# Kernel optimization log

Measured on AMD Instinct MI355X. Metric: run time of the kernel, lower is better.

The kernel has to match this reference:

```python
import jax, jax.numpy as jnp
import numpy as np

D_HIDDEN = 1024
N_HEADS = 16
D_HEAD = 64
B, N = 4, 1024
EPS = 1e-5


def _lin(x, w, b):
    # torch Linear: y = x @ W^T + b, w: [out, in]
    return jnp.einsum('...i,oi->...o', x, w) + b


def _ln(x, g, b):
    m = jnp.mean(x, axis=-1, keepdims=True)
    v = jnp.mean(jnp.square(x - m), axis=-1, keepdims=True)
    return (x - m) * jax.lax.rsqrt(v + EPS) * g + b


def setup_inputs() -> dict:
    key = jax.random.key(0)
    ks = jax.random.split(key, 20)
    d = D_HIDDEN
    s = 0.02
    inp = {
        'x': jax.random.normal(ks[0], (B, N, d), jnp.float32),
        'time_emb': jax.random.normal(ks[1], (B, d), jnp.float32),
        'ln1_g': jnp.ones((d,), jnp.float32),
        'ln1_b': jnp.zeros((d,), jnp.float32),
        's1_w': jax.random.normal(ks[2], (d, d), jnp.float32) * s,
        's1_b': jnp.zeros((d,), jnp.float32),
        'o1_w': jax.random.normal(ks[3], (d, d), jnp.float32) * s,
        'o1_b': jnp.zeros((d,), jnp.float32),
        'qkv_w': jax.random.normal(ks[4], (3 * d, d), jnp.float32) * s,
        'qkv_b': jnp.zeros((3 * d,), jnp.float32),
        'proj_w': jax.random.normal(ks[5], (d, d), jnp.float32) * s,
        'proj_b': jnp.zeros((d,), jnp.float32),
        'ln2_g': jnp.ones((d,), jnp.float32),
        'ln2_b': jnp.zeros((d,), jnp.float32),
        's2_w': jax.random.normal(ks[6], (d, d), jnp.float32) * s,
        's2_b': jnp.zeros((d,), jnp.float32),
        'o2_w': jax.random.normal(ks[7], (d, d), jnp.float32) * s,
        'o2_b': jnp.zeros((d,), jnp.float32),
        'up_w': jax.random.normal(ks[8], (4 * d, d), jnp.float32) * s,
        'up_b': jnp.zeros((4 * d,), jnp.float32),
        'down_w': jax.random.normal(ks[9], (d, 4 * d), jnp.float32) * s,
        'down_b': jnp.zeros((d,), jnp.float32),
    }
    return inp


def reference(x, time_emb, ln1_g, ln1_b, s1_w, s1_b, o1_w, o1_b,
              qkv_w, qkv_b, proj_w, proj_b, ln2_g, ln2_b,
              s2_w, s2_b, o2_w, o2_b, up_w, up_b, down_w, down_b):
    d = D_HIDDEN

    def ada(h, sw, sb, ow, ob):
        scale = _lin(time_emb, sw, sb)[:, None, :]   # [B,1,d]
        offset = _lin(time_emb, ow, ob)[:, None, :]
        return (1.0 + scale) * h + offset

    # attention branch
    h = ada(_ln(x, ln1_g, ln1_b), s1_w, s1_b, o1_w, o1_b)
    qkv = _lin(h, qkv_w, qkv_b)                       # [B,N,3d]
    q, k, v = jnp.split(qkv, 3, axis=-1)
    q = q.reshape(B, N, N_HEADS, D_HEAD)
    k = k.reshape(B, N, N_HEADS, D_HEAD)
    v = v.reshape(B, N, N_HEADS, D_HEAD)
    wei = jnp.einsum('bnhd,bmhd->bhnm', q, k) * (D_HEAD ** -0.5)
    wei = jax.nn.softmax(wei, axis=-1)
    attn = jnp.einsum('bhnm,bmhd->bnhd', wei, v).reshape(B, N, d)
    x = x + _lin(attn, proj_w, proj_b)

    # mlp branch (torch nn.GELU default = exact erf gelu)
    h = ada(_ln(x, ln2_g, ln2_b), s2_w, s2_b, o2_w, o2_b)
    h = jax.nn.gelu(_lin(h, up_w, up_b), approximate=False)
    x = x + _lin(h, down_w, down_b)
    return x, time_emb
```

## Files before the change

kernel.cpp:

```cpp
#include <hip/hip_runtime.h>
#include <hip/hip_bf16.h>
#include <math.h>

#define DH 1024
#define BB 4
#define NN 1024
#define NH 16
#define HD 64

typedef __attribute__((ext_vector_type(8))) short bf16x8;
typedef __attribute__((ext_vector_type(4))) float f32x4;
typedef unsigned short u16;

static __device__ __forceinline__ u16 f2bf(float f) {
  __hip_bfloat16 h = __float2bfloat16(f);
  return *reinterpret_cast<u16*>(&h);
}
static __device__ __forceinline__ float bf2f(u16 x) {
  return __uint_as_float((unsigned)x << 16);
}

#define MFMA16(a, b, c) __builtin_amdgcn_mfma_f32_16x16x32_bf16(a, b, c, 0, 0, 0)
#define VMCNT(n) asm volatile("s_waitcnt vmcnt(" #n ")" ::: "memory")
#define MEMFENCE asm volatile("" ::: "memory")

static __device__ __forceinline__ void async16(const void* g, void* l) {
  __builtin_amdgcn_global_load_lds(
      (const __attribute__((address_space(1))) void*)g,
      (__attribute__((address_space(3))) void*)l, 16, 0, 0);
}

__global__ void cvt_all_kernel(const float* __restrict__ wq, const float* __restrict__ wp,
                               const float* __restrict__ wu, const float* __restrict__ wd,
                               u16* __restrict__ oq, u16* __restrict__ op,
                               u16* __restrict__ ou, u16* __restrict__ od) {
  int i = blockIdx.x * 256 + threadIdx.x;
  const float* src; u16* dst; int off;
  if (i < 786432)            { src = wq; dst = oq; off = i; }
  else if (i < 1048576)      { src = wp; dst = op; off = i - 786432; }
  else if (i < 2097152)      { src = wu; dst = ou; off = i - 1048576; }
  else                       { src = wd; dst = od; off = i - 2097152; }
  float4 v = reinterpret_cast<const float4*>(src)[off];
  ushort4 o;
  o.x = f2bf(v.x); o.y = f2bf(v.y); o.z = f2bf(v.z); o.w = f2bf(v.w);
  reinterpret_cast<ushort4*>(dst)[off] = o;
}

__global__ __launch_bounds__(256) void adaln_kernel(
    const float* __restrict__ e,
    const float* __restrict__ w_s1, const float* __restrict__ b_s1,
    const float* __restrict__ w_o1, const float* __restrict__ b_o1,
    const float* __restrict__ w_s2, const float* __restrict__ b_s2,
    const float* __restrict__ w_o2, const float* __restrict__ b_o2,
    float* __restrict__ out) {
  int tid = threadIdx.x, wid = tid >> 6, lane = tid & 63;
  int mat = blockIdx.y;
  const float* w; const float* bs; float addc;
  if (mat == 0)      { w = w_s1; bs = b_s1; addc = 1.f; }
  else if (mat == 1) { w = w_o1; bs = b_o1; addc = 0.f; }
  else if (mat == 2) { w = w_s2; bs = b_s2; addc = 1.f; }
  else               { w = w_o2; bs = b_o2; addc = 0.f; }
  int col = blockIdx.x * 4 + wid;
  float a0 = 0.f, a1 = 0.f, a2 = 0.f, a3 = 0.f;
  const float* wc_ = w + (size_t)col * DH;
  for (int i = 0; i < 16; ++i) {
    int k = i * 64 + lane;
    float wv = wc_[k];
    a0 += wv * e[k];
    a1 += wv * e[DH + k];
    a2 += wv * e[2 * DH + k];
    a3 += wv * e[3 * DH + k];
  }
  #pragma unroll
  for (int msk = 32; msk; msk >>= 1) {
    a0 += __shfl_xor(a0, msk); a1 += __shfl_xor(a1, msk);
    a2 += __shfl_xor(a2, msk); a3 += __shfl_xor(a3, msk);
  }
  if (lane == 0) {
    float bb = bs[col] + addc;
    out[mat * (4 * DH) + 0 * DH + col] = a0 + bb;
    out[mat * (4 * DH) + 1 * DH + col] = a1 + bb;
    out[mat * (4 * DH) + 2 * DH + col] = a2 + bb;
    out[mat * (4 * DH) + 3 * DH + col] = a3 + bb;
  }
}

__global__ __launch_bounds__(256) void ln_mod_kernel(
    const float* __restrict__ x, const float* __restrict__ g, const float* __restrict__ bta,
    const float* __restrict__ sp, const float* __restrict__ off, u16* __restrict__ out) {
  int row = blockIdx.x;
  int b = row >> 10;
  int tid = threadIdx.x;
  int wid = tid >> 6, lane = tid & 63;
  const float4 xv = reinterpret_cast<const float4*>(x + (size_t)row * DH)[tid];
  float s = xv.x + xv.y + xv.z + xv.w;
  float ss = xv.x * xv.x + xv.y * xv.y + xv.z * xv.z + xv.w * xv.w;
  #pragma unroll
  for (int m = 32; m; m >>= 1) { s += __shfl_xor(s, m); ss += __shfl_xor(ss, m); }
  __shared__ float red[8];
  if (lane == 0) { red[wid] = s; red[4 + wid] = ss; }
  __syncthreads();
  s = red[0] + red[1] + red[2] + red[3];
  ss = red[4] + red[5] + red[6] + red[7];
  float mean = s * (1.f / DH);
  float var = ss * (1.f / DH) - mean * mean;
  float rstd = rsqrtf(var + 1e-5f);
  int c = tid * 4;
  const float* spb = sp + b * DH + c;
  const float* offb = off + b * DH + c;
  float y0 = (xv.x - mean) * rstd * g[c + 0] + bta[c + 0];
  float y1 = (xv.y - mean) * rstd * g[c + 1] + bta[c + 1];
  float y2 = (xv.z - mean) * rstd * g[c + 2] + bta[c + 2];
  float y3 = (xv.w - mean) * rstd * g[c + 3] + bta[c + 3];
  ushort4 o;
  o.x = f2bf(spb[0] * y0 + offb[0]);
  o.y = f2bf(spb[1] * y1 + offb[1]);
  o.z = f2bf(spb[2] * y2 + offb[2]);
  o.w = f2bf(spb[3] * y3 + offb[3]);
  reinterpret_cast<ushort4*>(out + (size_t)row * DH)[tid] = o;
}

enum { EPI_BF16 = 0, EPI_GELU = 1, EPI_PART = 2 };

template <int EPI>
__global__ __launch_bounds__(512, 2) void gemm256_kernel(
    const u16* __restrict__ A, const u16* __restrict__ W,
    const float* __restrict__ bias, void* __restrict__ outp,
    int N, int K, int KT) {
  extern __shared__ u16 lds[];
  u16* Ab = lds;
  u16* Bb = lds + 32768;
  int tid = threadIdx.x;
  int wid = tid >> 6, lane = tid & 63;
  int l15 = lane & 15, l4 = lane >> 4;
  int wr = wid >> 2, wc = wid & 3;

  int nwg = gridDim.x * gridDim.y;
  int lin = blockIdx.y * gridDim.x + blockIdx.x;
  int q8 = nwg >> 3;
  int lin2 = (lin & 7) * q8 + (lin >> 3);
  int bx = lin2 % gridDim.x, by = lin2 / gridDim.x;
  int m0 = by * 256, n0 = bx * 256;
  int k0 = blockIdx.z * (KT << 5);

  f32x4 acc[8][4] = {};

  const u16* Abase = A + (size_t)m0 * K + k0;
  const u16* Wbase = W + (size_t)n0 * K + k0;
  int i0 = tid, i1 = 512 + tid;
  int r0 = i0 >> 2, c0 = (i0 & 3) ^ ((r0 >> 1) & 3);
  int r1 = i1 >> 2, c1 = (i1 & 3) ^ ((r1 >> 1) & 3);
  size_t gO0 = (size_t)r0 * K + c0 * 8;
  size_t gO1 = (size_t)r1 * K + c1 * 8;
  int lb0 = (wid * 64) * 8;
  int lb1 = (512 + wid * 64) * 8;

  auto stage = [&](int tt) {
    int q = (tt & 3) * 8192;
    const u16* Ak = Abase + tt * 32;
    const u16* Wk = Wbase + tt * 32;
    async16(Ak + gO0, &Ab[q + lb0]);
    async16(Ak + gO1, &Ab[q + lb1]);
    async16(Wk + gO0, &Bb[q + lb0]);
    async16(Wk + gO1, &Bb[q + lb1]);
  };

  auto compute = [&](int tt) {
    int q = (tt & 3) * 8192;
    bf16x8 af[8], bfr[4];
    #pragma unroll
    for (int m = 0; m < 8; ++m) {
      int row = wr * 128 + m * 16 + l15;
      int ps = l4 ^ ((row >> 1) & 3);
      af[m] = *reinterpret_cast<const bf16x8*>(&Ab[q + row * 32 + ps * 8]);
    }
    #pragma unroll
    for (int n = 0; n < 4; ++n) {
      int row = wc * 64 + n * 16 + l15;
      int ps = l4 ^ ((row >> 1) & 3);
      bfr[n] = *reinterpret_cast<const bf16x8*>(&Bb[q + row * 32 + ps * 8]);
    }
    #pragma unroll
    for (int m = 0; m < 8; ++m)
      #pragma unroll
      for (int n = 0; n < 4; ++n)
        acc[m][n] = MFMA16(af[m], bfr[n], acc[m][n]);
  };

  stage(0);
  if (KT > 1) stage(1);
  if (KT > 2) stage(2);
  for (int t = 0; t < KT; ++t) {
    if (t < KT - 3) { stage(t + 3); VMCNT(12); }
    else if (t == KT - 3) { VMCNT(8); }
    else if (t == KT - 2) { VMCNT(4); }
    else { VMCNT(0); }
    __builtin_amdgcn_s_barrier();
    MEMFENCE;
    compute(t);
    MEMFENCE;
    __builtin_amdgcn_s_barrier();
  }

  int M = gridDim.y * 256;
  u16* pout = (u16*)outp + (size_t)blockIdx.z * M * N;
  #pragma unroll
  for (int n = 0; n < 4; ++n) {
    int col = n0 + wc * 64 + n * 16 + l15;
    float bv = (EPI == EPI_PART) ? 0.f : bias[col];
    #pragma unroll
    for (int m = 0; m < 8; ++m) {
      #pragma unroll
      for (int r = 0; r < 4; ++r) {
        int rowg = m0 + wr * 128 + m * 16 + l4 * 4 + r;
        float v = acc[m][n][r] + bv;
        if (EPI == EPI_GELU) {
          v = 0.5f * v * (1.f + erff(v * 0.70710678118f));
          ((u16*)outp)[(size_t)rowg * N + col] = f2bf(v);
        } else if (EPI == EPI_BF16) {
          ((u16*)outp)[(size_t)rowg * N + col] = f2bf(v);
        } else {
          pout[(size_t)rowg * N + col] = f2bf(v);
        }
      }
    }
  }
}

enum { OEPI_BF16 = 0, OEPI_GELU = 1, OEPI_RES = 2 };

template <int EPI>
__global__ __launch_bounds__(256, 3) void gemm_bt_kernel(
    const u16* __restrict__ A, const u16* __restrict__ W,
    const float* __restrict__ bias, const float* __restrict__ resid,
    void* __restrict__ outp, int N, int K) {
  __shared__ __align__(16) u16 As[2][128 * 32];
  __shared__ __align__(16) u16 Ws[2][128 * 32];
  int tid = threadIdx.x;
  int wid = tid >> 6, lane = tid & 63;
  int l15 = lane & 15, l4 = lane >> 4;
  int m0 = blockIdx.y * 128, n0 = blockIdx.x * 128;
  int wr = wid >> 1, wc = wid & 1;
  f32x4 acc[4][4] = {};

  const int KT = K >> 5;
  int idx0 = tid, idx1 = 256 + tid;
  int rowA0 = idx0 >> 2, gs0 = (idx0 & 3) ^ ((rowA0 >> 1) & 3);
  int rowA1 = idx1 >> 2, gs1 = (idx1 & 3) ^ ((rowA1 >> 1) & 3);
  const u16* Abase = A + (size_t)m0 * K;
  const u16* Wbase = W + (size_t)n0 * K;
  int lb0 = (wid * 64) * 8;
  int lb1 = (256 + wid * 64) * 8;

  auto stage = [&](int buf, int kt) {
    const u16* Ak = Abase + kt * 32;
    const u16* Wk = Wbase + kt * 32;
    async16(Ak + (size_t)rowA0 * K + gs0 * 8, &As[buf][lb0]);
    async16(Wk + (size_t)rowA0 * K + gs0 * 8, &Ws[buf][lb0]);
    async16(Ak + (size_t)rowA1 * K + gs1 * 8, &As[buf][lb1]);
    async16(Wk + (size_t)rowA1 * K + gs1 * 8, &Ws[buf][lb1]);
  };

  auto compute = [&](int buf) {
    bf16x8 af[4], wf[4];
    #pragma unroll
    for (int m = 0; m < 4; ++m) {
      int row = wr * 64 + m * 16 + l15;
      int ps = l4 ^ ((row >> 1) & 3);
      af[m] = *reinterpret_cast<const bf16x8*>(&As[buf][row * 32 + ps * 8]);
    }
    #pragma unroll
    for (int n = 0; n < 4; ++n) {
      int row = wc * 64 + n * 16 + l15;
      int ps = l4 ^ ((row >> 1) & 3);
      wf[n] = *reinterpret_cast<const bf16x8*>(&Ws[buf][row * 32 + ps * 8]);
    }
    #pragma unroll
    for (int m = 0; m < 4; ++m)
      #pragma unroll
      for (int n = 0; n < 4; ++n)
        acc[m][n] = MFMA16(af[m], wf[n], acc[m][n]);
  };

  stage(0, 0);
  __syncthreads();
  int buf = 0;
  for (int kt = 0; kt < KT - 1; ++kt) {
    stage(buf ^ 1, kt + 1);
    compute(buf);
    __syncthreads();
    buf ^= 1;
  }
  compute(buf);

  #pragma unroll
  for (int n = 0; n < 4; ++n) {
    int col = n0 + wc * 64 + n * 16 + l15;
    float bv = bias[col];
    #pragma unroll
    for (int m = 0; m < 4; ++m) {
      #pragma unroll
      for (int r = 0; r < 4; ++r) {
        int rowg = m0 + wr * 64 + m * 16 + l4 * 4 + r;
        float v = acc[m][n][r] + bv;
        if (EPI == OEPI_GELU) {
          v = 0.5f * v * (1.f + erff(v * 0.70710678118f));
          ((u16*)outp)[(size_t)rowg * N + col] = f2bf(v);
        } else if (EPI == OEPI_BF16) {
          ((u16*)outp)[(size_t)rowg * N + col] = f2bf(v);
        } else {
          ((float*)outp)[(size_t)rowg * N + col] = v + resid[(size_t)rowg * N + col];
        }
      }
    }
  }
}

__global__ __launch_bounds__(256) void reduce4_kernel(
    const u16* __restrict__ part, const float* __restrict__ x2,
    const float* __restrict__ bias, const float* __restrict__ te,
    float* __restrict__ out) {
  size_t i = (size_t)blockIdx.x * 256 + threadIdx.x;
  const size_t MN = (size_t)4096 * 1024;
  float4 xr = reinterpret_cast<const float4*>(x2)[i];
  int col = (int)((i * 4) & 1023);
  float4 bv = *reinterpret_cast<const float4*>(&bias[col]);
  float a0 = xr.x + bv.x, a1 = xr.y + bv.y, a2 = xr.z + bv.z, a3 = xr.w + bv.w;
  #pragma unroll
  for (int p = 0; p < 4; ++p) {
    ushort4 u = reinterpret_cast<const ushort4*>(part + p * MN)[i];
    a0 += bf2f(u.x); a1 += bf2f(u.y); a2 += bf2f(u.z); a3 += bf2f(u.w);
  }
  float4 o; o.x = a0; o.y = a1; o.z = a2; o.w = a3;
  reinterpret_cast<float4*>(out)[i] = o;
  if (blockIdx.x < 16) {
    int ii = blockIdx.x * 256 + threadIdx.x;
    out[4096 * 1024 + ii] = te[ii];
  }
}

__global__ __launch_bounds__(256) void vt_kernel(const u16* __restrict__ qkvb,
                                                 u16* __restrict__ vT) {
  __shared__ u16 L[64 * 66];
  int bh = blockIdx.y;
  int b = bh >> 4, h = bh & 15;
  int nt = blockIdx.x;
  int t = threadIdx.x;
  const u16* src = qkvb + ((size_t)b * 1024 + nt * 64) * 3072 + 2048 + h * 64;
  int j = t >> 3, s = t & 7;
  bf16x8 r0 = *reinterpret_cast<const bf16x8*>(src + (size_t)j * 3072 + s * 8);
  bf16x8 r1 = *reinterpret_cast<const bf16x8*>(src + (size_t)(j + 32) * 3072 + s * 8);
  #pragma unroll
  for (int e = 0; e < 8; ++e) {
    L[(s * 8 + e) * 66 + j] = r0[e];
    L[(s * 8 + e) * 66 + j + 32] = r1[e];
  }
  __syncthreads();
  int d = t & 63, cp = t >> 6;
  u16* dst = vT + ((size_t)bh * 64 + d) * 1024 + nt * 64;
  #pragma unroll
  for (int half = 0; half < 2; ++half) {
    int cs = cp + half * 4;
    bf16x8 o;
    #pragma unroll
    for (int c = 0; c < 8; ++c) o[c] = L[d * 66 + cs * 8 + c];
    *reinterpret_cast<bf16x8*>(dst + cs * 8) = o;
  }
}

__global__ __launch_bounds__(256, 4) void attn_kernel(
    const u16* __restrict__ qkv, const u16* __restrict__ vT, u16* __restrict__ out) {
  __shared__ __align__(16) u16 Ks[2][4096];
  __shared__ __align__(16) u16 Vs[2][4096];
  __shared__ __align__(16) u16 Ps[4][1024];
  int tid = threadIdx.x, wid = tid >> 6, lane = tid & 63;
  int l15 = lane & 15, l4 = lane >> 4;
  int L = blockIdx.y * gridDim.x + blockIdx.x;
  int qt = (L >> 3) & 15;
  int bh = (L & 7) | ((L >> 7) << 3);
  int b = bh >> 4, h = bh & 15;
  const size_t SN = 3 * DH;
  const u16* qb = qkv + (size_t)b * NN * SN + h * HD;
  const u16* kb = qb + DH;
  const u16* vtb = vT + (size_t)bh * 64 * 1024;

  int qrow = qt * 64 + wid * 16 + l15;
  bf16x8 qf[2];
  #pragma unroll
  for (int ks = 0; ks < 2; ++ks)
    qf[ks] = *reinterpret_cast<const bf16x8*>(qb + (size_t)qrow * SN + ks * 32 + l4 * 8);

  float m_[4], l_[4];
  f32x4 o_[4] = {};
  #pragma unroll
  for (int r = 0; r < 4; ++r) { m_[r] = -1e30f; l_[r] = 0.f; }

  int iA = tid, iB = 256 + tid;
  int jA = iA >> 3, sA = iA & 7, gsA = sA ^ (jA & 7);
  int jB = iB >> 3, sB = iB & 7, gsB = sB ^ (jB & 7);

  auto stageKV = [&](int bufn, int t) {
    const u16* kt = kb + (size_t)t * 64 * SN;
    async16(kt + (size_t)jA * SN + gsA * 8, &Ks[bufn][iA * 8]);
    async16(kt + (size_t)jB * SN + gsB * 8, &Ks[bufn][iB * 8]);
    const u16* vt = vtb + (size_t)t * 64;
    async16(vt + (size_t)jA * 1024 + gsA * 8, &Vs[bufn][iA * 8]);
    async16(vt + (size_t)jB * 1024 + gsB * 8, &Vs[bufn][iB * 8]);
  };

  stageKV(0, 0);
  __syncthreads();

  int buf = 0;
  for (int t = 0; t < 16; ++t) {
    if (t < 15) stageKV(buf ^ 1, t + 1);

    f32x4 sa[4];
    #pragma unroll
    for (int nb = 0; nb < 4; ++nb) {
      f32x4 s = {};
      #pragma unroll
      for (int ks = 0; ks < 2; ++ks) {
        int j = nb * 16 + l15;
        int ps = (ks * 4 + l4) ^ (j & 7);
        bf16x8 kf = *reinterpret_cast<const bf16x8*>(&Ks[buf][j * 64 + ps * 8]);
        s = MFMA16(qf[ks], kf, s);
      }
      sa[nb] = s * 0.125f;
    }

    float rm[4], tsum[4];
    #pragma unroll
    for (int r = 0; r < 4; ++r) {
      float v = fmaxf(fmaxf(sa[0][r], sa[1][r]), fmaxf(sa[2][r], sa[3][r]));
      #pragma unroll
      for (int msk = 1; msk < 16; msk <<= 1) v = fmaxf(v, __shfl_xor(v, msk));
      rm[r] = v;
    }
    float gmx = fmaxf(fmaxf(rm[0] - m_[0], rm[1] - m_[1]),
                      fmaxf(rm[2] - m_[2], rm[3] - m_[3]));
    if (!__all(gmx <= 8.f)) {
      #pragma unroll
      for (int r = 0; r < 4; ++r) {
        float mn = fmaxf(m_[r], rm[r]);
        float corr = __expf(m_[r] - mn);
        m_[r] = mn;
        l_[r] *= corr;
        #pragma unroll
        for (int nd = 0; nd < 4; ++nd) o_[nd][r] *= corr;
      }
    }
    #pragma unroll
    for (int r = 0; r < 4; ++r) tsum[r] = 0.f;
    #pragma unroll
    for (int nb = 0; nb < 4; ++nb) {
      #pragma unroll
      for (int r = 0; r < 4; ++r) {
        float p = __expf(sa[nb][r] - m_[r]);
        sa[nb][r] = p;
        tsum[r] += p;
      }
    }
    #pragma unroll
    for (int r = 0; r < 4; ++r) {
      float v = tsum[r];
      #pragma unroll
      for (int msk = 1; msk < 16; msk <<= 1) v += __shfl_xor(v, msk);
      l_[r] += v;
    }

    u16* Pw = Ps[wid];
    #pragma unroll
    for (int nb = 0; nb < 4; ++nb) {
      int slot = nb * 2 + (l15 >> 3);
      #pragma unroll
      for (int r = 0; r < 4; ++r) {
        int row = l4 * 4 + r;
        int ps = slot ^ (row & 7);
        Pw[row * 64 + ps * 8 + (l15 & 7)] = f2bf(sa[nb][r]);
      }
    }

    __builtin_amdgcn_s_setprio(1);
    #pragma unroll
    for (int ks = 0; ks < 2; ++ks) {
      int psp = (ks * 4 + l4) ^ (l15 & 7);
      bf16x8 pa = *reinterpret_cast<const bf16x8*>(&Pw[l15 * 64 + psp * 8]);
      #pragma unroll
      for (int nd = 0; nd < 4; ++nd) {
        int d = nd * 16 + l15;
        int psv = (ks * 4 + l4) ^ (d & 7);
        bf16x8 vf = *reinterpret_cast<const bf16x8*>(&Vs[buf][d * 64 + psv * 8]);
        o_[nd] = MFMA16(pa, vf, o_[nd]);
      }
    }
    __builtin_amdgcn_s_setprio(0);

    if (t < 15) __syncthreads();
    buf ^= 1;
  }

  float inv[4];
  #pragma unroll
  for (int r = 0; r < 4; ++r) inv[r] = 1.f / l_[r];
  u16* ob = out + (size_t)b * NN * DH + h * HD;
  #pragma unroll
  for (int nd = 0; nd < 4; ++nd) {
    #pragma unroll
    for (int r = 0; r < 4; ++r) {
      int q = qt * 64 + wid * 16 + l4 * 4 + r;
      ob[(size_t)q * DH + nd * 16 + l15] = f2bf(o_[nd][r] * inv[r]);
    }
  }
}

extern "C" void kernel_launch(void* const* d_in, const int* in_sizes, int n_in,
                              void* d_out, int out_size, void* d_ws, size_t ws_size,
                              hipStream_t stream) {
  (void)in_sizes; (void)n_in; (void)out_size; (void)ws_size;
  const float* x      = (const float*)d_in[0];
  const float* te     = (const float*)d_in[1];
  const float* ln1_g  = (const float*)d_in[2];
  const float* ln1_b  = (const float*)d_in[3];
  const float* s1_w   = (const float*)d_in[4];
  const float* s1_b   = (const float*)d_in[5];
  const float* o1_w   = (const float*)d_in[6];
  const float* o1_b   = (const float*)d_in[7];
  const float* qkv_w  = (const float*)d_in[8];
  const float* qkv_b  = (const float*)d_in[9];
  const float* proj_w = (const float*)d_in[10];
  const float* proj_b = (const float*)d_in[11];
  const float* ln2_g  = (const float*)d_in[12];
  const float* ln2_b  = (const float*)d_in[13];
  const float* s2_w   = (const float*)d_in[14];
  const float* s2_b   = (const float*)d_in[15];
  const float* o2_w   = (const float*)d_in[16];
  const float* o2_b   = (const float*)d_in[17];
  const float* up_w   = (const float*)d_in[18];
  const float* up_b   = (const float*)d_in[19];
  const float* down_w = (const float*)d_in[20];
  const float* down_b = (const float*)d_in[21];

  char* ws = (char*)d_ws;
  size_t off = 0;
  auto alloc = [&](size_t bytes) { void* p = ws + off; off += (bytes + 255) & ~255ull; return p; };
  u16*   wq   = (u16*)  alloc((size_t)3072 * 1024 * 2);
  u16*   wp   = (u16*)  alloc((size_t)1024 * 1024 * 2);
  u16*   wu   = (u16*)  alloc((size_t)4096 * 1024 * 2);
  u16*   h1   = (u16*)  alloc((size_t)4096 * 1024 * 2);
  u16*   qkvb = (u16*)  alloc((size_t)4096 * 3072 * 2);
  u16*   att  = (u16*)  alloc((size_t)4096 * 1024 * 2);
  u16*   h2   = (u16*)  alloc((size_t)4096 * 1024 * 2);
  u16*   wd   = (u16*)  alloc((size_t)1024 * 4096 * 2);
  float* x2   = (float*)alloc((size_t)4096 * 1024 * 4);
  u16*   upb  = (u16*)  alloc((size_t)4096 * 4096 * 2);
  float* ada  = (float*)alloc((size_t)4 * 4 * 1024 * 4);
  float* sp1 = ada, *off1 = ada + 4096, *sp2 = ada + 8192, *off2 = ada + 12288;
  u16*   part = wq;
  u16*   vT   = h1;

  cvt_all_kernel<<<12288, 256, 0, stream>>>(qkv_w, proj_w, up_w, down_w, wq, wp, wu, wd);
  adaln_kernel<<<dim3(256, 4), 256, 0, stream>>>(te, s1_w, s1_b, o1_w, o1_b, s2_w, s2_b, o2_w, o2_b, ada);
  ln_mod_kernel<<<4096, 256, 0, stream>>>(x, ln1_g, ln1_b, sp1, off1, h1);
  gemm256_kernel<EPI_BF16><<<dim3(12, 16, 1), 512, 131072, stream>>>(h1, wq, qkv_b, qkvb, 3072, 1024, 32);
  vt_kernel<<<dim3(16, 64), 256, 0, stream>>>(qkvb, vT);
  attn_kernel<<<dim3(16, 64), 256, 0, stream>>>(qkvb, vT, att);
  gemm_bt_kernel<OEPI_RES><<<dim3(8, 32), 256, 0, stream>>>(att, wp, proj_b, x, x2, 1024, 1024);
  ln_mod_kernel<<<4096, 256, 0, stream>>>(x2, ln2_g, ln2_b, sp2, off2, h2);
  gemm256_kernel<EPI_GELU><<<dim3(16, 16, 1), 512, 131072, stream>>>(h2, wu, up_b, upb, 4096, 1024, 32);
  gemm256_kernel<EPI_PART><<<dim3(4, 16, 4), 512, 131072, stream>>>(upb, wd, nullptr, part, 1024, 4096, 32);
  reduce4_kernel<<<4096, 256, 0, stream>>>(part, x2, down_b, te, (float*)d_out);
}
```

Measured before the change: 268.0 us.

## Split GEMM k-step into two halves interleaving A/B staging with MFMA

The GEMM main loop now splits each k-step into two half-phases. Each phase loads half the A fragments, issues async loads for the next A or B tile, syncs, then runs MFMAs at raised wave priority via s_setprio. This ping-pong schedule is meant to overlap global-to-LDS traffic and LDS reads with MFMA work, and to keep waves out of lockstep contention. It adds more barriers per iteration, and the vmcnt accounting is subtle, so hazards or extra sync overhead are possible.

```diff
diff --git a/kernel.cpp b/kernel.cpp
--- a/kernel.cpp
+++ b/kernel.cpp
@@ -23,6 +23,7 @@
 #define MFMA16(a, b, c) __builtin_amdgcn_mfma_f32_16x16x32_bf16(a, b, c, 0, 0, 0)
 #define VMCNT(n) asm volatile("s_waitcnt vmcnt(" #n ")" ::: "memory")
 #define MEMFENCE asm volatile("" ::: "memory")
+#define BAR() do { __builtin_amdgcn_s_barrier(); MEMFENCE; } while (0)
 
 static __device__ __forceinline__ void async16(const void* g, void* l) {
   __builtin_amdgcn_global_load_lds(
@@ -155,21 +156,30 @@
   int lb0 = (wid * 64) * 8;
   int lb1 = (512 + wid * 64) * 8;
 
-  auto stage = [&](int tt) {
+  auto stageA = [&](int tt) {
     int q = (tt & 3) * 8192;
     const u16* Ak = Abase + tt * 32;
-    const u16* Wk = Wbase + tt * 32;
     async16(Ak + gO0, &Ab[q + lb0]);
     async16(Ak + gO1, &Ab[q + lb1]);
+  };
+  auto stageB = [&](int tt) {
+    int q = (tt & 3) * 8192;
+    const u16* Wk = Wbase + tt * 32;
     async16(Wk + gO0, &Bb[q + lb0]);
     async16(Wk + gO1, &Bb[q + lb1]);
   };
 
-  auto compute = [&](int tt) {
-    int q = (tt & 3) * 8192;
+  stageA(0); stageB(0);
+  if (KT > 1) { stageA(1); stageB(1); }
+  if (KT > 2) { stageA(2); stageB(2); }
+  VMCNT(8);
+  BAR();
+
+  for (int t = 0; t < KT; ++t) {
+    int q = (t & 3) * 8192;
     bf16x8 af[8], bfr[4];
     #pragma unroll
-    for (int m = 0; m < 8; ++m) {
+    for (int m = 0; m < 4; ++m) {
       int row = wr * 128 + m * 16 + l15;
       int ps = l4 ^ ((row >> 1) & 3);
       af[m] = *reinterpret_cast<const bf16x8*>(&Ab[q + row * 32 + ps * 8]);
@@ -180,26 +190,36 @@
       int ps = l4 ^ ((row >> 1) & 3);
       bfr[n] = *reinterpret_cast<const bf16x8*>(&Bb[q + row * 32 + ps * 8]);
     }
-    #pragma unroll
-    for (int m = 0; m < 8; ++m)
+    if (t < KT - 3) stageA(t + 3);
+    BAR();
+    __builtin_amdgcn_s_setprio(1);
+    #pragma unroll
+    for (int m = 0; m < 4; ++m)
       #pragma unroll
       for (int n = 0; n < 4; ++n)
         acc[m][n] = MFMA16(af[m], bfr[n], acc[m][n]);
-  };
-
-  stage(0);
-  if (KT > 1) stage(1);
-  if (KT > 2) stage(2);
-  for (int t = 0; t < KT; ++t) {
-    if (t < KT - 3) { stage(t + 3); VMCNT(12); }
-    else if (t == KT - 3) { VMCNT(8); }
-    else if (t == KT - 2) { VMCNT(4); }
-    else { VMCNT(0); }
-    __builtin_amdgcn_s_barrier();
+    __builtin_amdgcn_s_setprio(0);
     MEMFENCE;
-    compute(t);
+    BAR();
+    #pragma unroll
+    for (int m = 4; m < 8; ++m) {
+      int row = wr * 128 + m * 16 + l15;
+      int ps = l4 ^ ((row >> 1) & 3);
+      af[m] = *reinterpret_cast<const bf16x8*>(&Ab[q + row * 32 + ps * 8]);
+    }
+    if (t < KT - 3) { stageB(t + 3); VMCNT(8); }
+    else if (t == KT - 3) { VMCNT(4); }
+    else if (t == KT - 2) { VMCNT(0); }
+    BAR();
+    __builtin_amdgcn_s_setprio(1);
+    #pragma unroll
+    for (int m = 4; m < 8; ++m)
+      #pragma unroll
+      for (int n = 0; n < 4; ++n)
+        acc[m][n] = MFMA16(af[m], bfr[n], acc[m][n]);
+    __builtin_amdgcn_s_setprio(0);
     MEMFENCE;
-    __builtin_amdgcn_s_barrier();
+    BAR();
   }
 
   int M = gridDim.y * 256;
```

After: 270.2 us. About the same (+0.8%).
